# Kernel tuning notes

Hardware: AMD Instinct MI355X
Metric: run time of the kernel (lower is better)

Reference implementation:

```python
import jax, jax.numpy as jnp
import numpy as np

B = 768
D = 128
NUM_CLASSES = 32
MARGIN = 1.0
EPS = 1e-12  # avoid sqrt(0) -> nan grad on the diagonal


def setup_inputs() -> dict:
    key = jax.random.key(0)
    k1, k2 = jax.random.split(key)
    embeddings = jax.random.normal(k1, (B, D), dtype=jnp.float32)
    labels = jax.random.randint(k2, (B,), 0, NUM_CLASSES, dtype=jnp.int32)
    return {"embeddings": embeddings, "labels": labels}


def _triplet_loss(embeddings, labels, margin):
    n = embeddings.shape[0]
    # pairwise euclidean distances (torch.cdist p=2)
    sq = jnp.sum(embeddings * embeddings, axis=1)
    d2 = sq[:, None] + sq[None, :] - 2.0 * (embeddings @ embeddings.T)
    d = jnp.sqrt(jnp.maximum(d2, EPS))  # [B, B]

    same = labels[:, None] == labels[None, :]
    eye = jnp.eye(n, dtype=bool)
    pos_mask = same & ~eye          # valid anchor-positive pairs
    neg_mask = ~same                # valid negatives per anchor
    neg_exists = neg_mask.any(axis=1)

    # hardest negative per anchor (argmin over negatives) -- fallback
    d_neg_only = jnp.where(neg_mask, d, jnp.inf)
    hardest = jnp.argmin(d_neg_only, axis=1)  # [B]

    # semi-hard mask[i, j, k]: k is negative of i and pd < d[i,k] < pd + margin
    pd = d[:, :, None]   # d[i, j]
    nd = d[:, None, :]   # d[i, k]
    semi = neg_mask[:, None, :] & (nd > pd) & (nd < pd + margin)  # [B,B,B] bool
    semi_any = semi.any(axis=2)                 # [B, B]
    first_semi = jnp.argmax(semi, axis=2)       # first True index, like negative_indices[mask][0]

    neg_idx = jnp.where(semi_any, first_semi, hardest[:, None])  # [B, B]
    neg_d = jnp.take_along_axis(d, neg_idx, axis=1)              # [B, B]

    valid = pos_mask & neg_exists[:, None]
    per_triplet = jax.nn.relu(d - neg_d + margin)  # relu(pos - neg + margin)
    cnt = jnp.sum(valid)
    loss = jnp.sum(jnp.where(valid, per_triplet, 0.0)) / jnp.maximum(cnt, 1).astype(per_triplet.dtype)
    return loss


def reference(embeddings, labels):
    return _triplet_loss(embeddings, labels, MARGIN)
```

## Files before the change

kernel.cpp:

```cpp
#include <hip/hip_runtime.h>
#include <math.h>

#define NB 768
#define ND 128
#define NC 12
#define APB 3
#define NTH 768
#define TL_MARGIN 1.0f
#define TL_EPS 1e-12f


__global__ __launch_bounds__(256) void transpose_kernel(
    const float* __restrict__ E, float* __restrict__ ET)
{
    const int b   = blockIdx.x;
    const int tid = threadIdx.x;
    const int k   = b / 3;
    const int j   = (b % 3) * 256 + tid;
    ET[(size_t)k * NB + j] = E[(size_t)j * ND + k];
}

__global__ __launch_bounds__(NTH) void triplet_fused_kernel(
    const float* __restrict__ E, const float* __restrict__ ET,
    const int* __restrict__ L,
    float* __restrict__ psum, float* __restrict__ pcnt)
{
    __shared__ float drow[APB][NB];

    const int tid  = threadIdx.x;
    const int lane = tid & 63;
    const int wave = tid >> 6;
    int i0 = blockIdx.x * APB;
    i0 = __builtin_amdgcn_readfirstlane(i0);

    const float* __restrict__ A0 = E + (size_t)(i0 + 0) * ND;
    const float* __restrict__ A1 = E + (size_t)(i0 + 1) * ND;
    const float* __restrict__ A2 = E + (size_t)(i0 + 2) * ND;

    float sqa = 0.f;
    if (wave < APB) {
        const float* __restrict__ Ar = E + (size_t)(i0 + wave) * ND;
        float v0 = Ar[lane], v1 = Ar[lane + 64];
        float s = v0 * v0 + v1 * v1;
        #pragma unroll
        for (int off = 32; off > 0; off >>= 1) s += __shfl_xor(s, off);
        sqa = s;
    }

    {
        const int j = wave * 64 + lane;
        const float* __restrict__ Bcol = ET + j;
        float p0 = 0.f, p1 = 0.f, p2 = 0.f, sjv = 0.f;
        #pragma unroll 16
        for (int k = 0; k < ND; ++k) {
            float b = Bcol[(size_t)k * NB];
            float a0 = A0[k], a1 = A1[k], a2 = A2[k];
            sjv += b * b;
            p0 += a0 * b; p1 += a1 * b; p2 += a2 * b;
        }
        drow[0][j] = sjv - 2.f * p0;
        drow[1][j] = sjv - 2.f * p1;
        drow[2][j] = sjv - 2.f * p2;
    }
    __syncthreads();

    if (wave < APB) {
        const int ia = i0 + wave;
        const int li = L[ia];
        unsigned negm = 0u, posm = 0u;
        float dk[NC];
        #pragma unroll
        for (int c = 0; c < NC; ++c) {
            int j = c * 64 + lane;
            dk[c] = sqrtf(fmaxf(sqa + drow[wave][j], TL_EPS));
            int lj = L[j];
            if (lj != li)     negm |= (1u << c);
            else if (j != ia) posm |= (1u << c);
        }

        float bv = INFINITY;
        #pragma unroll
        for (int c = 0; c < NC; ++c)
            if ((negm >> c) & 1u) bv = fminf(bv, dk[c]);
        #pragma unroll
        for (int off = 32; off > 0; off >>= 1)
            bv = fminf(bv, __shfl_xor(bv, off));
        const float hval = bv;

        float lsum = 0.f, lcnt = 0.f;
        if (isfinite(hval)) {
            #pragma unroll
            for (int c = 0; c < NC; ++c) {
                unsigned long long pm = __ballot((posm >> c) & 1u);
                while (pm) {
                    const int sl = __builtin_ctzll(pm);
                    pm &= pm - 1;
                    const float pd = __shfl(dk[c], sl);
                    float nd = hval;
                    #pragma unroll
                    for (int c2 = 0; c2 < NC; ++c2) {
                        bool pred = ((negm >> c2) & 1u) &&
                                    (dk[c2] > pd) && (dk[c2] < pd + TL_MARGIN);
                        unsigned long long m = __ballot(pred);
                        if (m) { nd = __shfl(dk[c2], __builtin_ctzll(m)); break; }
                    }
                    lsum += fmaxf(pd - nd + TL_MARGIN, 0.f);
                    lcnt += 1.f;
                }
            }
        }
        if (lane == 0) { psum[ia] = lsum; pcnt[ia] = lcnt; }
    }
}

__global__ __launch_bounds__(64) void triplet_finalize_kernel(
    const float* __restrict__ psum, const float* __restrict__ pcnt,
    float* __restrict__ out)
{
    const int lane = threadIdx.x;
    const float4* ps4 = (const float4*)psum;
    const float4* pc4 = (const float4*)pcnt;
    float a = 0.f, b = 0.f;
    #pragma unroll
    for (int r = 0; r < 3; ++r) {
        float4 x = ps4[lane + r * 64];
        float4 y = pc4[lane + r * 64];
        a += x.x + x.y + x.z + x.w;
        b += y.x + y.y + y.z + y.w;
    }
    #pragma unroll
    for (int off = 32; off > 0; off >>= 1) {
        a += __shfl_xor(a, off);
        b += __shfl_xor(b, off);
    }
    if (lane == 0) out[0] = a / fmaxf(b, 1.f);
}

extern "C" void kernel_launch(void* const* d_in, const int* in_sizes, int n_in,
                              void* d_out, int out_size, void* d_ws, size_t ws_size,
                              hipStream_t stream) {
    const float* E = (const float*)d_in[0];
    const int*   L = (const int*)d_in[1];
    char* ws = (char*)d_ws;
    float* ET   = (float*)(ws);
    float* psum = (float*)(ws + 0x60000);
    float* pcnt = (float*)(ws + 0x60C00);
    float* out  = (float*)d_out;

    transpose_kernel<<<NB * ND / 256, 256, 0, stream>>>(E, ET);
    triplet_fused_kernel<<<NB / APB, NTH, 0, stream>>>(E, ET, L, psum, pcnt);
    triplet_finalize_kernel<<<1, 64, 0, stream>>>(psum, pcnt, out);
}
```

Before: 27.07 us.

## Split dot-product K range and spread triplet mining across all waves

The Gram-row computation is restructured so each wave handles 128 columns over half the K dimension, using float2 loads. Two partial results are kept in shared memory and summed when the distances are formed. The semi-hard mining loop, which previously ran on only 3 of 12 waves, is now spread across all 12: each anchor's positive chunks are divided among 4 waves, and the per-wave sums are reduced through shared memory. This is meant to remove the serial bottleneck of idle waves during mining, at the cost of redundant distance computation per wave and an extra barrier.

```diff
diff --git a/kernel.cpp b/kernel.cpp
--- a/kernel.cpp
+++ b/kernel.cpp
@@ -25,7 +25,8 @@
     const int* __restrict__ L,
     float* __restrict__ psum, float* __restrict__ pcnt)
 {
-    __shared__ float drow[APB][NB];
+    __shared__ float drowp[2][APB][NB];
+    __shared__ float wsum[12], wcnt[12];
 
     const int tid  = threadIdx.x;
     const int lane = tid & 63;
@@ -37,42 +38,52 @@
     const float* __restrict__ A1 = E + (size_t)(i0 + 1) * ND;
     const float* __restrict__ A2 = E + (size_t)(i0 + 2) * ND;
 
-    float sqa = 0.f;
-    if (wave < APB) {
-        const float* __restrict__ Ar = E + (size_t)(i0 + wave) * ND;
-        float v0 = Ar[lane], v1 = Ar[lane + 64];
-        float s = v0 * v0 + v1 * v1;
-        #pragma unroll
-        for (int off = 32; off > 0; off >>= 1) s += __shfl_xor(s, off);
-        sqa = s;
-    }
-
     {
-        const int j = wave * 64 + lane;
-        const float* __restrict__ Bcol = ET + j;
-        float p0 = 0.f, p1 = 0.f, p2 = 0.f, sjv = 0.f;
+        const int h  = wave / 6;
+        const int jw = wave % 6;
+        const int j0 = jw * 128 + lane * 2;
+        const int k0 = h * 64;
+        const float2* __restrict__ Bcol = (const float2*)(ET + (size_t)k0 * NB + j0);
+        float p0x = 0.f, p0y = 0.f, p1x = 0.f, p1y = 0.f, p2x = 0.f, p2y = 0.f;
+        float sjx = 0.f, sjy = 0.f;
         #pragma unroll 16
-        for (int k = 0; k < ND; ++k) {
-            float b = Bcol[(size_t)k * NB];
+        for (int kk = 0; kk < 64; ++kk) {
+            float2 b = Bcol[(size_t)kk * (NB / 2)];
+            const int k = k0 + kk;
             float a0 = A0[k], a1 = A1[k], a2 = A2[k];
-            sjv += b * b;
-            p0 += a0 * b; p1 += a1 * b; p2 += a2 * b;
+            sjx += b.x * b.x; sjy += b.y * b.y;
+            p0x += a0 * b.x; p0y += a0 * b.y;
+            p1x += a1 * b.x; p1y += a1 * b.y;
+            p2x += a2 * b.x; p2y += a2 * b.y;
         }
-        drow[0][j] = sjv - 2.f * p0;
-        drow[1][j] = sjv - 2.f * p1;
-        drow[2][j] = sjv - 2.f * p2;
+        *(float2*)&drowp[h][0][j0] = make_float2(sjx - 2.f * p0x, sjy - 2.f * p0y);
+        *(float2*)&drowp[h][1][j0] = make_float2(sjx - 2.f * p1x, sjy - 2.f * p1y);
+        *(float2*)&drowp[h][2][j0] = make_float2(sjx - 2.f * p2x, sjy - 2.f * p2y);
     }
     __syncthreads();
 
-    if (wave < APB) {
-        const int ia = i0 + wave;
-        const int li = L[ia];
+    {
+        const int a    = wave % 3;
+        const int part = wave / 3;
+        const int ia   = i0 + a;
+        const int li   = L[ia];
+
+        float sqa;
+        {
+            const float* __restrict__ Ar = E + (size_t)ia * ND;
+            float v0 = Ar[lane], v1 = Ar[lane + 64];
+            float s = v0 * v0 + v1 * v1;
+            #pragma unroll
+            for (int off = 32; off > 0; off >>= 1) s += __shfl_xor(s, off);
+            sqa = s;
+        }
+
         unsigned negm = 0u, posm = 0u;
         float dk[NC];
         #pragma unroll
         for (int c = 0; c < NC; ++c) {
             int j = c * 64 + lane;
-            dk[c] = sqrtf(fmaxf(sqa + drow[wave][j], TL_EPS));
+            dk[c] = sqrtf(fmaxf(sqa + drowp[0][a][j] + drowp[1][a][j], TL_EPS));
             int lj = L[j];
             if (lj != li)     negm |= (1u << c);
             else if (j != ia) posm |= (1u << c);
@@ -90,7 +101,8 @@
         float lsum = 0.f, lcnt = 0.f;
         if (isfinite(hval)) {
             #pragma unroll
-            for (int c = 0; c < NC; ++c) {
+            for (int q = 0; q < 3; ++q) {
+                const int c = part + q * 4;
                 unsigned long long pm = __ballot((posm >> c) & 1u);
                 while (pm) {
                     const int sl = __builtin_ctzll(pm);
@@ -109,7 +121,12 @@
                 }
             }
         }
-        if (lane == 0) { psum[ia] = lsum; pcnt[ia] = lcnt; }
+        if (lane == 0) { wsum[wave] = lsum; wcnt[wave] = lcnt; }
+    }
+    __syncthreads();
+    if (tid < APB) {
+        psum[i0 + tid] = wsum[tid] + wsum[tid + 3] + wsum[tid + 6] + wsum[tid + 9];
+        pcnt[i0 + tid] = wcnt[tid] + wcnt[tid + 3] + wcnt[tid + 6] + wcnt[tid + 9];
     }
 }
 
```

Measured after the change: 28.58 us. +5.6%, slower.
